# Performance work log

Measured on AMD Instinct MI355X. Metric: run time of the kernel, lower is better.

The kernel has to match this reference:

```python
import jax, jax.numpy as jnp
import numpy as np

T = 0.2          # temperature
W = 0.1          # loss weight
BIG = 2 ** 30    # sentinel label for masked-out samples


def setup_inputs() -> dict:
    key = jax.random.key(0)
    k1, k2, k3, k4 = jax.random.split(key, 4)
    bs, C, Gn, S = 32, 128, 256, 16
    grouped_features = jax.random.normal(k1, (bs, C, Gn, S), dtype=jnp.float32)
    # instance labels in [-1, 8): -1 = background
    proposal_instance_mask = jax.random.randint(k2, (bs, Gn, S), -1, 8, dtype=jnp.int32)
    # seed indices with duplicates possible (range 40 over 16 samples)
    grouped_indices = jax.random.randint(k3, (bs, Gn, S), 0, 40, dtype=jnp.int32)
    context_compen = jax.random.normal(k4, (1, C), dtype=jnp.float32)
    return {
        "proposal_instance_mask": proposal_instance_mask,
        "grouped_features": grouped_features,
        "grouped_indices": grouped_indices,
        "context_compen": context_compen,
    }


def _group_loss(feat, idx, lab, ctx):
    # feat: [S, C], idx: [S], lab: [S], ctx: [C]
    # NOTE: sum_{a,b} f_a . g_b / (n_f * n_g) == mean(f) . mean(g), so the
    # original tiny-mm contrastive loss reduces to pairwise dots of per-instance means.
    S, C = feat.shape
    pos = jnp.arange(S)
    # unique count of seed indices -> truncate to first u samples (as in torch code)
    si = jnp.sort(idx)
    u = 1 + jnp.sum(si[1:] != si[:-1])
    valid = pos < u
    lab_m = jnp.where(valid, lab, BIG)
    # per-group unique labels (sorted), jit-friendly
    sl = jnp.sort(lab_m)
    new = jnp.concatenate([jnp.ones((1,), bool), sl[1:] != sl[:-1]])
    cid = jnp.cumsum(new) - 1                      # compact id of each sorted label
    uniq = jnp.full((S,), BIG, sl.dtype).at[cid].set(sl)
    n_labels = jnp.sum(new & (sl != BIG))          # number of distinct valid labels
    has_bg = uniq[0] == -1                         # -1 sorts first if present
    # per-instance mean features via segment scatter-add
    comp = jnp.searchsorted(uniq, lab_m)           # sample -> compact instance slot
    sums = jnp.zeros((S, C), feat.dtype).at[comp].add(jnp.where(valid[:, None], feat, 0.0))
    cnts = jnp.zeros((S,), feat.dtype).at[comp].add(valid.astype(feat.dtype))
    means = sums / jnp.maximum(cnts, 1.0)[:, None]
    hb = has_bg.astype(jnp.int32)
    fg_count = n_labels - hb
    inst_num = fg_count + 1                        # bg slot always present
    # row 0 = bg mean (or context_compen if no bg), rows 1.. = fg means
    gidx = jnp.clip(pos + hb - 1, 0, S - 1)
    M = means[gidx]
    M = M.at[0].set(jnp.where(has_bg, M[0], ctx))
    inst_valid = pos < inst_num
    sim = (M @ M.T) / T                            # [S, S] tiny matmul of means
    sim_m = jnp.where(inst_valid[None, :], sim, -jnp.inf)
    lse = jax.scipy.special.logsumexp(sim_m, axis=1)
    li = lse - jnp.diagonal(sim)                   # -log(pos/(pos+neg)) per fg row
    fg_mask = inst_valid & (pos >= 1)
    gl = jnp.sum(jnp.where(fg_mask, li, 0.0)) / jnp.maximum(inst_num - 1, 1).astype(feat.dtype)
    return gl, fg_count >= 1


def reference(proposal_instance_mask, grouped_features, grouped_indices, context_compen):
    bs, C, Gn, S = grouped_features.shape
    feats = grouped_features.transpose(0, 2, 3, 1).reshape(-1, S, C)  # [G, S, C]
    idxs = grouped_indices.reshape(-1, S)
    labs = proposal_instance_mask.reshape(-1, S)
    ctx = context_compen[0]
    gl, gv = jax.vmap(lambda f, i, l: _group_loss(f, i, l, ctx))(feats, idxs, labs)
    gvf = gv.astype(gl.dtype)
    return jnp.sum(gl * gvf) / jnp.sum(gvf) * W
```

## Files before the change

kernel.cpp:

```cpp
#include <hip/hip_runtime.h>

#define GQ   8192
#define WPB  2
#define SQRT5 2.23606797749978969f

template<int CTRL>
__device__ __forceinline__ float dpp_add(float v) {
    int t = __builtin_amdgcn_update_dpp(0, __float_as_int(v), CTRL, 0xF, 0xF, true);
    return v + __int_as_float(t);
}
__device__ __forceinline__ float wave_sum64(float v) {
    v = dpp_add<0x111>(v);
    v = dpp_add<0x112>(v);
    v = dpp_add<0x114>(v);
    v = dpp_add<0x118>(v);
    v = dpp_add<0x142>(v);
    v = dpp_add<0x143>(v);
    return v;
}

__global__ __launch_bounds__(64 * WPB, 6) void group_loss_kernel(
    const int*   __restrict__ labs,
    const float* __restrict__ feats,
    const int*   __restrict__ idxs,
    const float* __restrict__ ctx,
    float2* __restrict__ ws)
{
    const int l  = threadIdx.x & 63;
    const int wu = threadIdx.x >> 6;
    const int blk = blockIdx.x;
    const int g  = ((blk & 7) << 10) | ((blk >> 3) << 1) | wu;
    const int b  = g >> 8;
    const int gn = g & 255;
    const long fbase = (long)b * (128 * 256 * 16) + (long)gn * 16;

    const float* gp0 = feats + fbase + (long)l * 4096;
    const float* gp1 = gp0 + 64 * 4096;
    float4 A[4], B[4];
    #pragma unroll
    for (int q = 0; q < 4; ++q) A[q] = *(const float4*)(gp0 + q * 4);
    #pragma unroll
    for (int q = 0; q < 4; ++q) B[q] = *(const float4*)(gp1 + q * 4);
    const float cx0 = ctx[l], cx1 = ctx[l + 64];

    int myidx = -1, mylab = -2;
    if (l < 16) { myidx = idxs[g * 16 + l]; mylab = labs[g * 16 + l]; }

    unsigned long long mm = ~0ull;
    #pragma unroll
    for (int bit = 0; bit < 6; ++bit) {
        const unsigned long long bb = __ballot((myidx >> bit) & 1);
        mm &= ((myidx >> bit) & 1) ? bb : ~bb;
    }
    const bool dup = (mm & ((1ull << l) - 1) & 0xFFFFull) != 0ull;
    const int u = __popcll(__ballot((l < 16) && !dup));

    const bool valid = l < u;
    const int bid = valid ? (mylab + 1) : 255;

    int cnt[9];
    #pragma unroll
    for (int r = 0; r < 9; ++r) cnt[r] = __popcll(__ballot(bid == r));
    const bool has_bg = cnt[0] > 0;
    int fg_count = 0, pm = 0;
    #pragma unroll
    for (int r = 1; r < 9; ++r)
        if (cnt[r] > 0) { ++fg_count; pm |= 1 << r; }

    float fa[16], fb[16];
    #pragma unroll
    for (int q = 0; q < 4; ++q) {
        fa[4*q+0] = A[q].x; fa[4*q+1] = A[q].y; fa[4*q+2] = A[q].z; fa[4*q+3] = A[q].w;
        fb[4*q+0] = B[q].x; fb[4*q+1] = B[q].y; fb[4*q+2] = B[q].z; fb[4*q+3] = B[q].w;
    }

    float m0[9] = {0,0,0,0,0,0,0,0,0};
    float m1[9] = {0,0,0,0,0,0,0,0,0};
    #pragma unroll
    for (int s = 0; s < 16; ++s) {
        if (s < u) {
            const int bs = __builtin_amdgcn_readlane(bid, s);
            switch (bs) {
                case 0: m0[0] += fa[s]; m1[0] += fb[s]; break;
                case 1: m0[1] += fa[s]; m1[1] += fb[s]; break;
                case 2: m0[2] += fa[s]; m1[2] += fb[s]; break;
                case 3: m0[3] += fa[s]; m1[3] += fb[s]; break;
                case 4: m0[4] += fa[s]; m1[4] += fb[s]; break;
                case 5: m0[5] += fa[s]; m1[5] += fb[s]; break;
                case 6: m0[6] += fa[s]; m1[6] += fb[s]; break;
                case 7: m0[7] += fa[s]; m1[7] += fb[s]; break;
                case 8: m0[8] += fa[s]; m1[8] += fb[s]; break;
            }
        }
    }
    #pragma unroll
    for (int r = 0; r < 9; ++r) {
        const float sc = SQRT5 / (float)(cnt[r] > 0 ? cnt[r] : 1);
        m0[r] *= sc; m1[r] *= sc;
    }
    if (!has_bg) { m0[0] = cx0 * SQRT5; m1[0] = cx1 * SQRT5; }

    const int PI_[44] = {1,1, 2,2,2, 3,3,3,3, 4,4,4,4,4, 5,5,5,5,5,5,
                         6,6,6,6,6,6,6, 7,7,7,7,7,7,7,7, 8,8,8,8,8,8,8,8,8};
    const int PJ_[44] = {0,1, 0,1,2, 0,1,2,3, 0,1,2,3,4, 0,1,2,3,4,5,
                         0,1,2,3,4,5,6, 0,1,2,3,4,5,6,7, 0,1,2,3,4,5,6,7,8};
    float pv[44];
    #pragma unroll
    for (int k = 0; k < 44; ++k)
        pv[k] = m0[PI_[k]] * m0[PJ_[k]] + m1[PI_[k]] * m1[PJ_[k]];
    #pragma unroll
    for (int k = 0; k < 44; ++k) pv[k] = wave_sum64(pv[k]);

    const int cm = pm | 1;
    int svi[44];
    #pragma unroll
    for (int k = 0; k < 44; ++k) {
        const int s = __builtin_amdgcn_readlane(__float_as_int(pv[k]), 63);
        const bool keep = (((cm >> PI_[k]) & 1) != 0) && (((cm >> PJ_[k]) & 1) != 0);
        svi[k] = keep ? s : 0xFF800000;
    }
    const int OFF_[9] = {0, 0, 2, 5, 9, 14, 20, 27, 35};
    #define SK(i, j) __int_as_float(svi[((i) >= (j)) ? (OFF_[(i)] + (j)) : (OFF_[(j)] + (i))])

    float ssum = 0.0f;
    #pragma unroll
    for (int r = 1; r < 9; ++r) {
        if ((pm >> r) & 1) {
            float vmax = SK(r, 0);
            #pragma unroll
            for (int j = 1; j < 9; ++j) vmax = fmaxf(vmax, SK(r, j));
            float se = 0.0f;
            #pragma unroll
            for (int j = 0; j < 9; ++j) se += __expf(SK(r, j) - vmax);
            ssum += vmax + __logf(se) - SK(r, r);
        }
    }

    if (l == 0) {
        float2 r;
        r.x = ssum / (float)(fg_count > 0 ? fg_count : 1);
        r.y = (fg_count > 0) ? 1.0f : 0.0f;
        ws[g] = r;
    }
    #undef SK
}

__global__ __launch_bounds__(1024) void reduce_kernel(
    const float2* __restrict__ ws, float* __restrict__ out)
{
    __shared__ float sa[1024], sb[1024];
    const int t = threadIdx.x;
    float a = 0.0f, b2 = 0.0f;
    for (int g = t; g < GQ; g += 1024) {
        float2 v = ws[g];
        a += v.x; b2 += v.y;
    }
    sa[t] = a; sb[t] = b2;
    __syncthreads();
    for (int off = 512; off > 0; off >>= 1) {
        if (t < off) { sa[t] += sa[t + off]; sb[t] += sb[t + off]; }
        __syncthreads();
    }
    if (t == 0) out[0] = 0.1f * (sa[0] / sb[0]);
}

extern "C" void kernel_launch(void* const* d_in, const int* in_sizes, int n_in,
                              void* d_out, int out_size, void* d_ws, size_t ws_size,
                              hipStream_t stream) {
    const int*   labs  = (const int*)d_in[0];
    const float* feats = (const float*)d_in[1];
    const int*   idxs  = (const int*)d_in[2];
    const float* ctx   = (const float*)d_in[3];
    float* out = (float*)d_out;
    float2* ws = (float2*)d_ws;

    group_loss_kernel<<<GQ / WPB, 64 * WPB, 0, stream>>>(labs, feats, idxs, ctx, ws);
    reduce_kernel<<<1, 1024, 0, stream>>>(ws, out);
}
```

Before: 116.1 us.

## Stage eight adjacent groups' features through LDS for coalesced global loads

Each block now handles 8 consecutive groups with one wave per group. The waves cooperatively load contiguous 512-byte feature rows per channel into padded shared memory, then each wave reads its own group's 16 samples back from LDS. Before, each lane issued strided 64-byte loads per channel, so the goal is fully coalesced global reads. The pairwise dot product and wave reduction are also merged into one loop to lower register pressure. In exchange it adds about 67 KB of LDS per block and a block-wide barrier, which cuts occupancy, and it drops the previous interleaved block-to-group mapping.

```diff
diff --git a/kernel.cpp b/kernel.cpp
--- a/kernel.cpp
+++ b/kernel.cpp
@@ -1,7 +1,8 @@
 #include <hip/hip_runtime.h>
 
-#define GQ   8192
-#define WPB  2
+#define GQ    8192
+#define BLKG  8
+#define MROW  132
 #define SQRT5 2.23606797749978969f
 
 template<int CTRL>
@@ -19,32 +20,38 @@
     return v;
 }
 
-__global__ __launch_bounds__(64 * WPB, 6) void group_loss_kernel(
+__global__ __launch_bounds__(64 * BLKG, 4) void group_loss_kernel(
     const int*   __restrict__ labs,
     const float* __restrict__ feats,
     const int*   __restrict__ idxs,
     const float* __restrict__ ctx,
     float2* __restrict__ ws)
 {
+    __shared__ float SH[128 * MROW];
+
     const int l  = threadIdx.x & 63;
-    const int wu = threadIdx.x >> 6;
-    const int blk = blockIdx.x;
-    const int g  = ((blk & 7) << 10) | ((blk >> 3) << 1) | wu;
-    const int b  = g >> 8;
-    const int gn = g & 255;
-    const long fbase = (long)b * (128 * 256 * 16) + (long)gn * 16;
-
-    const float* gp0 = feats + fbase + (long)l * 4096;
-    const float* gp1 = gp0 + 64 * 4096;
-    float4 A[4], B[4];
-    #pragma unroll
-    for (int q = 0; q < 4; ++q) A[q] = *(const float4*)(gp0 + q * 4);
-    #pragma unroll
-    for (int q = 0; q < 4; ++q) B[q] = *(const float4*)(gp1 + q * 4);
-    const float cx0 = ctx[l], cx1 = ctx[l + 64];
+    const int w  = threadIdx.x >> 6;
+    const int g0 = blockIdx.x * BLKG;
+    const int g  = g0 + w;
+    const int b  = g0 >> 8;
+    const int gn0 = g0 & 255;
 
     int myidx = -1, mylab = -2;
     if (l < 16) { myidx = idxs[g * 16 + l]; mylab = labs[g * 16 + l]; }
+    const float cx0 = ctx[l], cx1 = ctx[l + 64];
+
+    {
+        const int half = l >> 5;
+        const int lo   = l & 31;
+        const float* base = feats + (long)b * 524288 + (long)gn0 * 16;
+        #pragma unroll
+        for (int k = 0; k < 8; ++k) {
+            const int c = k * 16 + w * 2 + half;
+            const float4 v = *(const float4*)(base + (long)c * 4096 + lo * 4);
+            *(float4*)(SH + c * MROW + lo * 4) = v;
+        }
+    }
+    __syncthreads();
 
     unsigned long long mm = ~0ull;
     #pragma unroll
@@ -68,10 +75,16 @@
         if (cnt[r] > 0) { ++fg_count; pm |= 1 << r; }
 
     float fa[16], fb[16];
-    #pragma unroll
-    for (int q = 0; q < 4; ++q) {
-        fa[4*q+0] = A[q].x; fa[4*q+1] = A[q].y; fa[4*q+2] = A[q].z; fa[4*q+3] = A[q].w;
-        fb[4*q+0] = B[q].x; fb[4*q+1] = B[q].y; fb[4*q+2] = B[q].z; fb[4*q+3] = B[q].w;
+    {
+        const float* Ra = SH + l * MROW + w * 16;
+        const float* Rb = SH + (l + 64) * MROW + w * 16;
+        #pragma unroll
+        for (int q = 0; q < 4; ++q) {
+            const float4 x = *(const float4*)(Ra + 4 * q);
+            const float4 y = *(const float4*)(Rb + 4 * q);
+            fa[4*q+0] = x.x; fa[4*q+1] = x.y; fa[4*q+2] = x.z; fa[4*q+3] = x.w;
+            fb[4*q+0] = y.x; fb[4*q+1] = y.y; fb[4*q+2] = y.z; fb[4*q+3] = y.w;
+        }
     }
 
     float m0[9] = {0,0,0,0,0,0,0,0,0};
@@ -104,18 +117,13 @@
                          6,6,6,6,6,6,6, 7,7,7,7,7,7,7,7, 8,8,8,8,8,8,8,8,8};
     const int PJ_[44] = {0,1, 0,1,2, 0,1,2,3, 0,1,2,3,4, 0,1,2,3,4,5,
                          0,1,2,3,4,5,6, 0,1,2,3,4,5,6,7, 0,1,2,3,4,5,6,7,8};
-    float pv[44];
-    #pragma unroll
-    for (int k = 0; k < 44; ++k)
-        pv[k] = m0[PI_[k]] * m0[PJ_[k]] + m1[PI_[k]] * m1[PJ_[k]];
-    #pragma unroll
-    for (int k = 0; k < 44; ++k) pv[k] = wave_sum64(pv[k]);
-
     const int cm = pm | 1;
     int svi[44];
     #pragma unroll
     for (int k = 0; k < 44; ++k) {
-        const int s = __builtin_amdgcn_readlane(__float_as_int(pv[k]), 63);
+        float pv = m0[PI_[k]] * m0[PJ_[k]] + m1[PI_[k]] * m1[PJ_[k]];
+        pv = wave_sum64(pv);
+        const int s = __builtin_amdgcn_readlane(__float_as_int(pv), 63);
         const bool keep = (((cm >> PI_[k]) & 1) != 0) && (((cm >> PJ_[k]) & 1) != 0);
         svi[k] = keep ? s : 0xFF800000;
     }
@@ -135,6 +143,7 @@
             ssum += vmax + __logf(se) - SK(r, r);
         }
     }
+    #undef SK
 
     if (l == 0) {
         float2 r;
@@ -142,7 +151,6 @@
         r.y = (fg_count > 0) ? 1.0f : 0.0f;
         ws[g] = r;
     }
-    #undef SK
 }
 
 __global__ __launch_bounds__(1024) void reduce_kernel(
@@ -174,6 +182,6 @@
     float* out = (float*)d_out;
     float2* ws = (float2*)d_ws;
 
-    group_loss_kernel<<<GQ / WPB, 64 * WPB, 0, stream>>>(labs, feats, idxs, ctx, ws);
+    group_loss_kernel<<<GQ / BLKG, 64 * BLKG, 0, stream>>>(labs, feats, idxs, ctx, ws);
     reduce_kernel<<<1, 1024, 0, stream>>>(ws, out);
 }
```

Measured after the change: 115.1 us. About the same (-0.9%).
